# Kernel optimization log

Hardware: AMD Instinct MI355X
Metric: run time of the kernel (lower is better)

## Reference

```python
import jax, jax.numpy as jnp
import numpy as np

DIM = 384
NUM_HEADS = 12
WS = 8            # window_size
SS = 4            # shift_size
HEAD_DIM = DIM // NUM_HEADS
SCALE = HEAD_DIM ** -0.5
N = WS * WS       # tokens per window
EPS = 1e-5
MLP_HIDDEN = 4 * DIM

# relative position index (static, matches torch buffer construction)
_coords = np.stack(np.meshgrid(np.arange(WS), np.arange(WS), indexing='ij')).reshape(2, -1)
_rel = (_coords[:, :, None] - _coords[:, None, :]).transpose(1, 2, 0)  # [N,N,2]
_rel[..., 0] += WS - 1
_rel[..., 1] += WS - 1
_rel[..., 0] *= 2 * WS - 1
RPI = jnp.asarray(_rel.sum(-1))  # [N,N] int


def layer_norm(x, g, b):
    m = x.mean(-1, keepdims=True)
    v = ((x - m) ** 2).mean(-1, keepdims=True)
    return (x - m) / jnp.sqrt(v + EPS) * g + b


def window_partition(x):
    B, Hh, Ww, C = x.shape
    x = x.reshape(B, Hh // WS, WS, Ww // WS, WS, C).transpose(0, 1, 3, 2, 4, 5)
    return x.reshape(-1, WS, WS, C)


def window_reverse(w, Hh, Ww):
    B = w.shape[0] // ((Hh // WS) * (Ww // WS))
    x = w.reshape(B, Hh // WS, Ww // WS, WS, WS, -1).transpose(0, 1, 3, 2, 4, 5)
    return x.reshape(B, Hh, Ww, -1)


def attention_mask(Hp, Wp):
    # region id along each axis: 0 = [0, Hp-WS), 1 = [Hp-WS, Hp-SS), 2 = [Hp-SS, Hp)
    h_id = np.zeros(Hp, np.int32); h_id[Hp - WS:Hp - SS] = 1; h_id[Hp - SS:] = 2
    w_id = np.zeros(Wp, np.int32); w_id[Wp - WS:Wp - SS] = 1; w_id[Wp - SS:] = 2
    cnt = h_id[:, None] * 3 + w_id[None, :]                      # [Hp, Wp]
    img = jnp.asarray(cnt, jnp.float32).reshape(1, Hp, Wp, 1)
    mw = window_partition(img).reshape(-1, N)                    # [nW, N]
    am = mw[:, None, :] - mw[:, :, None]                         # [nW, N, N]
    return jnp.where(am != 0, jnp.float32(-100.0), jnp.float32(0.0))


def setup_inputs() -> dict:
    key = jax.random.key(0)
    ks = jax.random.split(key, 8)
    B, H, W = 32, 64, 64
    std = 0.02
    return {
        'x': jax.random.normal(ks[0], (B, H * W, DIM), jnp.float32),
        'qkv_w': jax.random.normal(ks[1], (DIM, 3 * DIM), jnp.float32) * std,
        'qkv_b': jnp.zeros((3 * DIM,), jnp.float32),
        'proj_w': jax.random.normal(ks[2], (DIM, DIM), jnp.float32) * std,
        'proj_b': jnp.zeros((DIM,), jnp.float32),
        'rpb_table': jax.random.normal(ks[3], ((2 * WS - 1) * (2 * WS - 1), NUM_HEADS), jnp.float32) * std,
        'n1_g': jnp.ones((DIM,), jnp.float32), 'n1_b': jnp.zeros((DIM,), jnp.float32),
        'n2_g': jnp.ones((DIM,), jnp.float32), 'n2_b': jnp.zeros((DIM,), jnp.float32),
        'fc1_w': jax.random.normal(ks[4], (DIM, MLP_HIDDEN), jnp.float32) * std,
        'fc1_b': jnp.zeros((MLP_HIDDEN,), jnp.float32),
        'fc2_w': jax.random.normal(ks[5], (MLP_HIDDEN, DIM), jnp.float32) * std,
        'fc2_b': jnp.zeros((DIM,), jnp.float32),
        'H': 64, 'W': 64,
    }


def reference(x, qkv_w, qkv_b, proj_w, proj_b, rpb_table, n1_g, n1_b, n2_g, n2_b,
              fc1_w, fc1_b, fc2_w, fc2_b, H, W):
    B, L, C = x.shape
    shortcut = x
    h = layer_norm(x, n1_g, n1_b).reshape(B, H, W, C)
    pad_r = (WS - W % WS) % WS
    pad_b = (WS - H % WS) % WS
    if pad_r or pad_b:
        h = jnp.pad(h, ((0, 0), (0, pad_b), (0, pad_r), (0, 0)))
    Hp, Wp = H + pad_b, W + pad_r
    shifted = jnp.roll(h, shift=(-SS, -SS), axis=(1, 2))
    xw = window_partition(shifted).reshape(-1, N, C)             # [B_, N, C]
    B_ = xw.shape[0]

    qkv = (xw @ qkv_w + qkv_b).reshape(B_, N, 3, NUM_HEADS, HEAD_DIM)
    q = qkv[:, :, 0].transpose(0, 2, 1, 3) * SCALE               # [B_, h, N, d]
    k = qkv[:, :, 1].transpose(0, 2, 1, 3)
    v = qkv[:, :, 2].transpose(0, 2, 1, 3)

    attn = jnp.einsum('bhnd,bhmd->bhnm', q, k)                   # [B_, h, N, N]
    bias = rpb_table[RPI].transpose(2, 0, 1)                     # [h, N, N]
    attn = attn + bias[None]

    mask = attention_mask(Hp, Wp)                                # [nW, N, N]
    nW = mask.shape[0]
    attn = attn.reshape(B_ // nW, nW, NUM_HEADS, N, N) + mask[None, :, None]
    attn = jax.nn.softmax(attn.reshape(B_, NUM_HEADS, N, N), axis=-1)

    out = jnp.einsum('bhnm,bhmd->bhnd', attn, v)
    out = out.transpose(0, 2, 1, 3).reshape(B_, N, C)
    out = out @ proj_w + proj_b

    out = window_reverse(out.reshape(-1, WS, WS, C), Hp, Wp)
    out = jnp.roll(out, shift=(SS, SS), axis=(1, 2))
    out = out[:, :H, :W, :].reshape(B, H * W, C)

    x = shortcut + out
    h2 = layer_norm(x, n2_g, n2_b)
    mlp = jax.nn.gelu(h2 @ fc1_w + fc1_b, approximate=False) @ fc2_w + fc2_b
    return x + mlp
```

## Files before the change

kernel.cpp:

```cpp
#include <hip/hip_runtime.h>
#include <math.h>


#define ROWS_TOTAL 131072
#define NWIN_TOTAL 2048

typedef __attribute__((ext_vector_type(8))) __bf16 bf16x8;
typedef __attribute__((ext_vector_type(4))) float f32x4;
typedef __attribute__((ext_vector_type(8))) unsigned short ushort8;

__device__ __forceinline__ unsigned short f2bf(float f) {
  unsigned u = __builtin_bit_cast(unsigned, f);
  u = (u + 0x7fffu + ((u >> 16) & 1u)) >> 16;
  return (unsigned short)u;
}
__device__ __forceinline__ float bf2f(unsigned short u) {
  return __builtin_bit_cast(float, (unsigned)u << 16);
}

__device__ __forceinline__ void gload16(const void* g, void* l) {
  __builtin_amdgcn_global_load_lds(
      (const __attribute__((address_space(1))) unsigned int*)g,
      (__attribute__((address_space(3))) unsigned int*)l, 16, 0, 0);
}

__device__ __forceinline__ int gather_row(int win, int t) {
  int b = win >> 6, wi = (win >> 3) & 7, wj = win & 7;
  int gi = (wi * 8 + (t >> 3) + 4) & 63;
  int gj = (wj * 8 + (t & 7) + 4) & 63;
  return (b << 12) + (gi << 6) + gj;
}

__device__ __forceinline__ float gelu_f(float v) {
  float x = v * 0.70710678118654752f;
  float ax = fabsf(x);
  float t = 1.f / (1.f + 0.3275911f * ax);
  float poly =
      t * (0.254829592f +
           t * (-0.284496736f +
                t * (1.421413741f + t * (-1.453152027f + t * 1.061405429f))));
  float er = 1.f - poly * __expf(-x * x);
  er = copysignf(er, x);
  return 0.5f * v * (1.f + er);
}

#define STG(buf_, t_)                                                   \
  {                                                                     \
    size_t ko = (size_t)(t_) * 64;                                      \
    gload16(aS0 + ko, (char*)As + (buf_) * 8192 + tid * 16);            \
    gload16(aS1 + ko, (char*)As + (buf_) * 8192 + 4096 + tid * 16);     \
    gload16(bS0 + ko, (char*)Bs + (buf_) * 6144 + tid * 16);            \
    if (tid < 128)                                                      \
      gload16(bS1 + ko, (char*)Bs + (buf_) * 6144 + 4096 + tid * 16);   \
  }

#define GEMM_DECLS()                                                    \
  f32x4 acc[4][3];                                                      \
  _Pragma("unroll") for (int i_ = 0; i_ < 4; ++i_)                      \
  _Pragma("unroll") for (int j_ = 0; j_ < 3; ++j_)                      \
      acc[i_][j_] = (f32x4)(0.f);                                       \
  int aO[4], bO[3];                                                     \
  _Pragma("unroll") for (int mi_ = 0; mi_ < 4; ++mi_) {                 \
    int row_ = wr * 64 + mi_ * 16 + lr;                                 \
    aO[mi_] = row_ * 32 + (((hi + (row_ >> 1)) & 3) << 3);              \
  }                                                                     \
  _Pragma("unroll") for (int nj_ = 0; nj_ < 3; ++nj_) {                 \
    int row_ = wc * 48 + nj_ * 16 + lr;                                 \
    bO[nj_] = row_ * 32 + (((hi + (row_ >> 1)) & 3) << 3);              \
  }

#define GEMM_CORE(NT_)                                                  \
  {                                                                     \
    int cur = 0;                                                        \
    STG(0, 0);                                                          \
    __syncthreads();                                                    \
    for (int t = 0; t < (NT_); ++t) {                                   \
      if (t + 1 < (NT_)) STG(cur ^ 1, t + 1);                           \
      const ushort* AsC = &As[cur][0];                                  \
      const ushort* BsC = &Bs[cur][0];                                  \
      bf16x8 bv[3];                                                     \
      _Pragma("unroll") for (int nj = 0; nj < 3; ++nj)                  \
          bv[nj] = *(const bf16x8*)(BsC + bO[nj]);                      \
      _Pragma("unroll") for (int mi = 0; mi < 4; ++mi) {                \
        bf16x8 av = *(const bf16x8*)(AsC + aO[mi]);                     \
        _Pragma("unroll") for (int nj = 0; nj < 3; ++nj)                \
          acc[mi][nj] = __builtin_amdgcn_mfma_f32_16x16x32_bf16(        \
              av, bv[nj], acc[mi][nj], 0, 0, 0);                        \
      }                                                                 \
      __syncthreads();                                                  \
      cur ^= 1;                                                         \
    }                                                                   \
  }

#define GRID_SWZ(NP_)                                                   \
  int p, bm;                                                            \
  {                                                                     \
    int lin = blockIdx.y * (NP_) + blockIdx.x;                          \
    if ((gridDim.y & 7) == 0) {                                         \
      int xcd = lin & 7, q = lin >> 3;                                  \
      p = q % (NP_); bm = (q / (NP_)) * 8 + xcd;                        \
    } else { p = blockIdx.x; bm = blockIdx.y; }                         \
  }

#define SRC_SWZ(t_) (((((t_) & 3) - (((t_) >> 3) & 3)) & 3) << 4)

__global__ __launch_bounds__(256) void wprep_k(
    const float* __restrict__ qkvw, const float* __restrict__ projw,
    const float* __restrict__ fc1w, const float* __restrict__ fc2w,
    ushort* __restrict__ wq, ushort* __restrict__ wp,
    ushort* __restrict__ w1, ushort* __restrict__ w2) {
  int gid = blockIdx.x * 256 + threadIdx.x;
  const int S1 = 1152 * 384;
  const int S2 = S1 + 384 * 384;
  const int S3 = S2 + 1536 * 384;
  const int S4 = S3 + 384 * 1536;
  if (gid < S1) {
    int n = gid / 384, k = gid - n * 384;
    wq[gid] = f2bf(qkvw[(size_t)k * 1152 + n]);
  } else if (gid < S2) {
    int i = gid - S1, n = i / 384, k = i - n * 384;
    wp[i] = f2bf(projw[(size_t)k * 384 + n]);
  } else if (gid < S3) {
    int i = gid - S2, n = i / 384, k = i - n * 384;
    w1[i] = f2bf(fc1w[(size_t)k * 1536 + n]);
  } else if (gid < S4) {
    int i = gid - S3, n = i / 1536, k = i - n * 1536;
    w2[i] = f2bf(fc2w[(size_t)k * 384 + n]);
  }
}

__global__ __launch_bounds__(256) void ln_fused_k(
    const float* __restrict__ x, const float* __restrict__ g,
    const float* __restrict__ b, ushort* __restrict__ o) {
  int wid = threadIdx.x >> 6, lane = threadIdx.x & 63;
  int row = (blockIdx.x << 2) + wid;
  const float* p = x + (size_t)row * 384;
  float2 v[3];
  float s = 0.f, ss = 0.f;
#pragma unroll
  for (int c = 0; c < 3; ++c) {
    v[c] = *(const float2*)(p + lane * 2 + c * 128);
    s += v[c].x + v[c].y;
    ss += v[c].x * v[c].x + v[c].y * v[c].y;
  }
#pragma unroll
  for (int off = 1; off < 64; off <<= 1) {
    s += __shfl_xor(s, off);
    ss += __shfl_xor(ss, off);
  }
  float m = s * (1.f / 384.f);
  float r = rsqrtf(ss * (1.f / 384.f) - m * m + 1e-5f);
  ushort* op = o + (size_t)row * 384;
#pragma unroll
  for (int c = 0; c < 3; ++c) {
    float2 gg = *(const float2*)(g + lane * 2 + c * 128);
    float2 bb = *(const float2*)(b + lane * 2 + c * 128);
    union { ushort u[2]; unsigned w; } pk;
    pk.u[0] = f2bf((v[c].x - m) * r * gg.x + bb.x);
    pk.u[1] = f2bf((v[c].y - m) * r * gg.y + bb.y);
    *(unsigned*)(op + lane * 2 + c * 128) = pk.w;
  }
}

__global__ __launch_bounds__(256) void qkv_mfma_k(
    const ushort* __restrict__ xln, const ushort* __restrict__ wq,
    const float* __restrict__ qkvb, ushort* __restrict__ qd,
    ushort* __restrict__ kd, ushort* __restrict__ vd, int wc0) {
  __shared__ __align__(16) ushort As[2][4096];
  __shared__ __align__(16) ushort Bs[2][3072];
  const int tid = threadIdx.x;
  const int lane = tid & 63;
  const int w = tid >> 6;
  const int wr = w >> 1, wc = w & 1;
  const int lr = lane & 15, hi = lane >> 4;
  GRID_SWZ(12);
  const int n0 = p * 96;
  int r0 = tid >> 2, r1 = (256 + tid) >> 2;
  const char* aS0 = (const char*)xln +
                    (size_t)gather_row(wc0 + bm * 2 + (r0 >> 6), r0 & 63) * 768 +
                    SRC_SWZ(tid);
  const char* aS1 = (const char*)xln +
                    (size_t)gather_row(wc0 + bm * 2 + (r1 >> 6), r1 & 63) * 768 +
                    SRC_SWZ(tid);
  const char* bS0 = (const char*)wq + (size_t)(n0 + (tid >> 2)) * 768 +
                    SRC_SWZ(tid);
  const char* bS1 = (const char*)wq + (size_t)(n0 + 64 + (tid >> 2)) * 768 +
                    SRC_SWZ(tid);
  GEMM_DECLS();
  GEMM_CORE(12);
  const float scale = 0.17677669529663687f;
#pragma unroll
  for (int mi = 0; mi < 4; ++mi) {
#pragma unroll
    for (int r = 0; r < 4; ++r) {
      int rr = wr * 64 + mi * 16 + (hi << 2) + r;
      int w_rel = bm * 2 + (rr >> 6), t = rr & 63;
#pragma unroll
      for (int nj = 0; nj < 3; ++nj) {
        int nc = n0 + wc * 48 + nj * 16 + lr;
        float v = acc[mi][nj][r] + qkvb[nc];
        int qi = nc / 384, rem = nc - qi * 384;
        int hh = rem >> 5, d = rem & 31;
        ushort* base = (qi == 0) ? qd : (qi == 1 ? kd : vd);
        if (qi == 0) v *= scale;
        base[(((size_t)w_rel * 12 + hh) << 11) + (t << 5) + d] = f2bf(v);
      }
    }
  }
}

__global__ __launch_bounds__(128) void attn_k(
    const ushort* __restrict__ q, const ushort* __restrict__ k,
    const ushort* __restrict__ v, const float* __restrict__ rpb,
    ushort* __restrict__ ao, int wc0) {
  __shared__ __align__(16) float kbuf[2][64][32];
  __shared__ __align__(16) float vbuf[2][64][32];
  __shared__ float bias[2][232];
  __shared__ int region[64];
  const int tid = threadIdx.x;
  const int wid = tid >> 6, lane = tid & 63;
  const int w = blockIdx.x, win = wc0 + w;
  const int head = blockIdx.y * 2 + wid;
  if (tid < 64) {
    int wi = (win >> 3) & 7, wj = win & 7;
    int pi = wi * 8 + (tid >> 3), pj = wj * 8 + (tid & 7);
    int ri = pi < 56 ? 0 : (pi < 60 ? 1 : 2);
    int rj = pj < 56 ? 0 : (pj < 60 ? 1 : 2);
    region[tid] = ri * 3 + rj;
  }
  const size_t hb = ((size_t)w * 12 + head) * 2048;
  const ushort* kp = k + hb;
  const ushort* vp = v + hb;
#pragma unroll
  for (int s = 0; s < 4; ++s) {
    int f = s * 64 + lane;
    int r = f >> 2, c = (f & 3) * 8;
    ushort8 ku = *(const ushort8*)(kp + r * 32 + c);
    ushort8 vu = *(const ushort8*)(vp + r * 32 + c);
#pragma unroll
    for (int j = 0; j < 8; ++j) {
      kbuf[wid][r][c + j] = bf2f(ku[j]);
      vbuf[wid][r][c + j] = bf2f(vu[j]);
    }
  }
  for (int s = lane; s < 225; s += 64) bias[wid][s] = rpb[s * 12 + head];
  __syncthreads();
  const int i = lane;
  float qr[32];
  const ushort* qp = q + hb + (i << 5);
#pragma unroll
  for (int c = 0; c < 4; ++c) {
    ushort8 qu = *(const ushort8*)(qp + c * 8);
#pragma unroll
    for (int j = 0; j < 8; ++j) qr[c * 8 + j] = bf2f(qu[j]);
  }
  const int yi = i >> 3, xi = i & 7, regi = region[i];
  float sc[64];
  float mx = -3.0e38f;
#pragma unroll
  for (int j = 0; j < 64; ++j) {
    float a = 0.f;
#pragma unroll
    for (int c = 0; c < 32; c += 4) {
      float4 kv = *(float4*)&kbuf[wid][j][c];
      a = fmaf(qr[c], kv.x, a);
      a = fmaf(qr[c + 1], kv.y, a);
      a = fmaf(qr[c + 2], kv.z, a);
      a = fmaf(qr[c + 3], kv.w, a);
    }
    int dy = yi - (j >> 3) + 7, dx = xi - (j & 7) + 7;
    a += bias[wid][dy * 15 + dx];
    if (region[j] != regi) a -= 100.f;
    sc[j] = a;
    mx = fmaxf(mx, a);
  }
  float sum = 0.f;
#pragma unroll
  for (int j = 0; j < 64; ++j) {
    float e = __expf(sc[j] - mx);
    sc[j] = e;
    sum += e;
  }
  const float inv = 1.f / sum;
  float o[32];
#pragma unroll
  for (int c = 0; c < 32; ++c) o[c] = 0.f;
#pragma unroll
  for (int j = 0; j < 64; ++j) {
    float p = sc[j];
#pragma unroll
    for (int c = 0; c < 32; c += 4) {
      float4 vv = *(float4*)&vbuf[wid][j][c];
      o[c] = fmaf(p, vv.x, o[c]);
      o[c + 1] = fmaf(p, vv.y, o[c + 1]);
      o[c + 2] = fmaf(p, vv.z, o[c + 2]);
      o[c + 3] = fmaf(p, vv.w, o[c + 3]);
    }
  }
  ushort* op = ao + ((size_t)(w * 64 + i)) * 384 + (head << 5);
#pragma unroll
  for (int c = 0; c < 32; c += 8) {
    ushort8 pk;
#pragma unroll
    for (int j2 = 0; j2 < 8; ++j2) pk[j2] = f2bf(o[c + j2] * inv);
    *(ushort8*)(op + c) = pk;
  }
}

__global__ __launch_bounds__(256) void proj_mfma_k(
    const ushort* __restrict__ ao, const ushort* __restrict__ wp,
    const float* __restrict__ pb, const float* __restrict__ x,
    float* __restrict__ x2, int wc0) {
  __shared__ __align__(16) ushort As[2][4096];
  __shared__ __align__(16) ushort Bs[2][3072];
  const int tid = threadIdx.x;
  const int lane = tid & 63;
  const int w = tid >> 6;
  const int wr = w >> 1, wc = w & 1;
  const int lr = lane & 15, hi = lane >> 4;
  GRID_SWZ(4);
  const int n0 = p * 96;
  const char* aS0 = (const char*)ao +
                    (size_t)(bm * 128 + (tid >> 2)) * 768 + SRC_SWZ(tid);
  const char* aS1 = (const char*)ao +
                    (size_t)(bm * 128 + 64 + (tid >> 2)) * 768 + SRC_SWZ(tid);
  const char* bS0 = (const char*)wp + (size_t)(n0 + (tid >> 2)) * 768 +
                    SRC_SWZ(tid);
  const char* bS1 = (const char*)wp + (size_t)(n0 + 64 + (tid >> 2)) * 768 +
                    SRC_SWZ(tid);
  GEMM_DECLS();
  GEMM_CORE(12);
#pragma unroll
  for (int mi = 0; mi < 4; ++mi) {
#pragma unroll
    for (int r = 0; r < 4; ++r) {
      int rr = wr * 64 + mi * 16 + (hi << 2) + r;
      int gl = bm * 128 + rr;
      int gr = gather_row(wc0 + (gl >> 6), gl & 63);
#pragma unroll
      for (int nj = 0; nj < 3; ++nj) {
        int nc = n0 + wc * 48 + nj * 16 + lr;
        size_t idx = (size_t)gr * 384 + nc;
        x2[idx] = acc[mi][nj][r] + pb[nc] + x[idx];
      }
    }
  }
}

__global__ __launch_bounds__(256) void fc1_mfma_k(
    const ushort* __restrict__ x2ln, const ushort* __restrict__ w1,
    const float* __restrict__ fb, ushort* __restrict__ hm, int row0) {
  __shared__ __align__(16) ushort As[2][4096];
  __shared__ __align__(16) ushort Bs[2][3072];
  const int tid = threadIdx.x;
  const int lane = tid & 63;
  const int w = tid >> 6;
  const int wr = w >> 1, wc = w & 1;
  const int lr = lane & 15, hi = lane >> 4;
  GRID_SWZ(16);
  const int n0 = p * 96;
  const char* aS0 = (const char*)x2ln +
                    (size_t)(row0 + bm * 128 + (tid >> 2)) * 768 +
                    SRC_SWZ(tid);
  const char* aS1 = (const char*)x2ln +
                    (size_t)(row0 + bm * 128 + 64 + (tid >> 2)) * 768 +
                    SRC_SWZ(tid);
  const char* bS0 = (const char*)w1 + (size_t)(n0 + (tid >> 2)) * 768 +
                    SRC_SWZ(tid);
  const char* bS1 = (const char*)w1 + (size_t)(n0 + 64 + (tid >> 2)) * 768 +
                    SRC_SWZ(tid);
  GEMM_DECLS();
  GEMM_CORE(12);
#pragma unroll
  for (int mi = 0; mi < 4; ++mi) {
#pragma unroll
    for (int r = 0; r < 4; ++r) {
      int rr = wr * 64 + mi * 16 + (hi << 2) + r;
      size_t lrow = (size_t)(bm * 128 + rr);
#pragma unroll
      for (int nj = 0; nj < 3; ++nj) {
        int nc = n0 + wc * 48 + nj * 16 + lr;
        float v = gelu_f(acc[mi][nj][r] + fb[nc]);
        hm[lrow * 1536 + nc] = f2bf(v);
      }
    }
  }
}

__global__ __launch_bounds__(256) void fc2_mfma_k(
    const ushort* __restrict__ hm, const ushort* __restrict__ w2,
    const float* __restrict__ fb, float* __restrict__ out, int row0) {
  __shared__ __align__(16) ushort As[2][4096];
  __shared__ __align__(16) ushort Bs[2][3072];
  const int tid = threadIdx.x;
  const int lane = tid & 63;
  const int w = tid >> 6;
  const int wr = w >> 1, wc = w & 1;
  const int lr = lane & 15, hi = lane >> 4;
  GRID_SWZ(4);
  const int n0 = p * 96;
  const char* aS0 = (const char*)hm +
                    (size_t)(bm * 128 + (tid >> 2)) * 3072 + SRC_SWZ(tid);
  const char* aS1 = (const char*)hm +
                    (size_t)(bm * 128 + 64 + (tid >> 2)) * 3072 +
                    SRC_SWZ(tid);
  const char* bS0 = (const char*)w2 + (size_t)(n0 + (tid >> 2)) * 3072 +
                    SRC_SWZ(tid);
  const char* bS1 = (const char*)w2 + (size_t)(n0 + 64 + (tid >> 2)) * 3072 +
                    SRC_SWZ(tid);
  GEMM_DECLS();
  GEMM_CORE(48);
#pragma unroll
  for (int mi = 0; mi < 4; ++mi) {
#pragma unroll
    for (int r = 0; r < 4; ++r) {
      int rr = wr * 64 + mi * 16 + (hi << 2) + r;
      size_t grow = (size_t)(row0 + bm * 128 + rr);
#pragma unroll
      for (int nj = 0; nj < 3; ++nj) {
        int nc = n0 + wc * 48 + nj * 16 + lr;
        size_t idx = grow * 384 + nc;
        out[idx] = out[idx] + acc[mi][nj][r] + fb[nc];
      }
    }
  }
}

extern "C" void kernel_launch(void* const* d_in, const int* in_sizes, int n_in,
                              void* d_out, int out_size, void* d_ws, size_t ws_size,
                              hipStream_t stream) {
  const float* x = (const float*)d_in[0];
  const float* qkv_w = (const float*)d_in[1];
  const float* qkv_b = (const float*)d_in[2];
  const float* proj_w = (const float*)d_in[3];
  const float* proj_b = (const float*)d_in[4];
  const float* rpb = (const float*)d_in[5];
  const float* n1g = (const float*)d_in[6];
  const float* n1b = (const float*)d_in[7];
  const float* n2g = (const float*)d_in[8];
  const float* n2b = (const float*)d_in[9];
  const float* fc1w = (const float*)d_in[10];
  const float* fc1b = (const float*)d_in[11];
  const float* fc2w = (const float*)d_in[12];
  const float* fc2b = (const float*)d_in[13];
  float* out = (float*)d_out;
  char* ws = (char*)d_ws;

  ushort* wq = (ushort*)ws;
  ushort* wp = wq + 442368;
  ushort* w1 = wp + 147456;
  ushort* w2 = w1 + 589824;
  ushort* xln = (ushort*)(ws + 3538944);
  char* scratch = ws + 3538944 + 100663296;
  size_t base = 3538944 + 100663296;
  size_t ssz = (ws_size > base) ? ws_size - base : 0;

  wprep_k<<<6912, 256, 0, stream>>>(qkv_w, proj_w, fc1w, fc2w, wq, wp, w1, w2);
  ln_fused_k<<<ROWS_TOTAL / 4, 256, 0, stream>>>(x, n1g, n1b, xln);

  const size_t perwin = 196608;
  int nwc = (int)(ssz / perwin);
  if (nwc > NWIN_TOTAL) nwc = NWIN_TOTAL;
  nwc &= ~31;
  if (nwc < 32) nwc = 32;
  ushort* qd = (ushort*)scratch;
  ushort* kd = qd + (size_t)nwc * 24576;
  ushort* vd = kd + (size_t)nwc * 24576;
  ushort* ao = vd + (size_t)nwc * 24576;
  for (int wc0 = 0; wc0 < NWIN_TOTAL; wc0 += nwc) {
    int nw = (NWIN_TOTAL - wc0 < nwc) ? (NWIN_TOTAL - wc0) : nwc;
    qkv_mfma_k<<<dim3(12, nw / 2), 256, 0, stream>>>(xln, wq, qkv_b, qd, kd,
                                                     vd, wc0);
    attn_k<<<dim3(nw, 6), 128, 0, stream>>>(qd, kd, vd, rpb, ao, wc0);
    proj_mfma_k<<<dim3(4, nw / 2), 256, 0, stream>>>(ao, wp, proj_b, x, out,
                                                     wc0);
  }

  ln_fused_k<<<ROWS_TOTAL / 4, 256, 0, stream>>>(out, n2g, n2b, xln);
  const size_t pergrp = 393216;
  int ngc = (int)(ssz / pergrp);
  if (ngc > 1024) ngc = 1024;
  ngc &= ~7;
  if (ngc < 8) ngc = 8;
  ushort* hm = (ushort*)scratch;
  for (int g0 = 0; g0 < 1024; g0 += ngc) {
    int ng = (1024 - g0 < ngc) ? (1024 - g0) : ngc;
    fc1_mfma_k<<<dim3(16, ng), 256, 0, stream>>>(xln, w1, fc1b, hm, g0 * 128);
    fc2_mfma_k<<<dim3(4, ng), 256, 0, stream>>>(hm, w2, fc2b, out, g0 * 128);
  }
}
```

Measured before the change: 1.552 ms.

## Switch GEMMs to 32x32x16 MFMA with 128x192 block tiles

All four GEMM kernels (qkv, proj, fc1, fc2) move from 16x16x32 MFMA to 32x32x16 MFMA with 16-float accumulators. The block N tile doubles from 96 to 192 columns, so B staging in LDS grows and the grid's N dimension is halved. The goal is higher arithmetic intensity per LDS read and fewer A-tile reloads across N blocks. In exchange there is more LDS per block and more accumulator registers, which may lower occupancy, and the epilogues now use a different output row mapping.

```diff
diff --git a/kernel.cpp b/kernel.cpp
--- a/kernel.cpp
+++ b/kernel.cpp
@@ -6,7 +6,7 @@
 #define NWIN_TOTAL 2048
 
 typedef __attribute__((ext_vector_type(8))) __bf16 bf16x8;
-typedef __attribute__((ext_vector_type(4))) float f32x4;
+typedef __attribute__((ext_vector_type(16))) float f32x16;
 typedef __attribute__((ext_vector_type(8))) unsigned short ushort8;
 
 __device__ __forceinline__ unsigned short f2bf(float f) {
@@ -44,29 +44,37 @@
   return 0.5f * v * (1.f + er);
 }
 
+#define SRC_SWZ(t_) (((((t_) & 3) - (((t_) >> 3) & 3)) & 3) << 4)
+
 #define STG(buf_, t_)                                                   \
   {                                                                     \
     size_t ko = (size_t)(t_) * 64;                                      \
     gload16(aS0 + ko, (char*)As + (buf_) * 8192 + tid * 16);            \
     gload16(aS1 + ko, (char*)As + (buf_) * 8192 + 4096 + tid * 16);     \
-    gload16(bS0 + ko, (char*)Bs + (buf_) * 6144 + tid * 16);            \
-    if (tid < 128)                                                      \
-      gload16(bS1 + ko, (char*)Bs + (buf_) * 6144 + 4096 + tid * 16);   \
+    gload16(bS0 + ko, (char*)Bs + (buf_) * 12288 + tid * 16);           \
+    gload16(bS1 + ko, (char*)Bs + (buf_) * 12288 + 4096 + tid * 16);    \
+    gload16(bS2 + ko, (char*)Bs + (buf_) * 12288 + 8192 + tid * 16);    \
   }
 
 #define GEMM_DECLS()                                                    \
-  f32x4 acc[4][3];                                                      \
-  _Pragma("unroll") for (int i_ = 0; i_ < 4; ++i_)                      \
+  f32x16 acc[2][3];                                                     \
+  _Pragma("unroll") for (int i_ = 0; i_ < 2; ++i_)                      \
   _Pragma("unroll") for (int j_ = 0; j_ < 3; ++j_)                      \
-      acc[i_][j_] = (f32x4)(0.f);                                       \
-  int aO[4], bO[3];                                                     \
-  _Pragma("unroll") for (int mi_ = 0; mi_ < 4; ++mi_) {                 \
-    int row_ = wr * 64 + mi_ * 16 + lr;                                 \
-    aO[mi_] = row_ * 32 + (((hi + (row_ >> 1)) & 3) << 3);              \
+      acc[i_][j_] = (f32x16)(0.f);                                      \
+  int aO[2][2], bO[3][2];                                               \
+  _Pragma("unroll") for (int mi_ = 0; mi_ < 2; ++mi_) {                 \
+    int row_ = wr * 64 + mi_ * 32 + (lane & 31);                        \
+    _Pragma("unroll") for (int sl_ = 0; sl_ < 2; ++sl_) {               \
+      int g_ = sl_ * 2 + (lane >> 5);                                   \
+      aO[mi_][sl_] = row_ * 32 + (((g_ + (row_ >> 1)) & 3) << 3);       \
+    }                                                                   \
   }                                                                     \
   _Pragma("unroll") for (int nj_ = 0; nj_ < 3; ++nj_) {                 \
-    int row_ = wc * 48 + nj_ * 16 + lr;                                 \
-    bO[nj_] = row_ * 32 + (((hi + (row_ >> 1)) & 3) << 3);              \
+    int row_ = wc * 96 + nj_ * 32 + (lane & 31);                        \
+    _Pragma("unroll") for (int sl_ = 0; sl_ < 2; ++sl_) {               \
+      int g_ = sl_ * 2 + (lane >> 5);                                   \
+      bO[nj_][sl_] = row_ * 32 + (((g_ + (row_ >> 1)) & 3) << 3);       \
+    }                                                                   \
   }
 
 #define GEMM_CORE(NT_)                                                  \
@@ -78,15 +86,18 @@
       if (t + 1 < (NT_)) STG(cur ^ 1, t + 1);                           \
       const ushort* AsC = &As[cur][0];                                  \
       const ushort* BsC = &Bs[cur][0];                                  \
-      bf16x8 bv[3];                                                     \
+      bf16x8 av[2][2], bv[3][2];                                        \
+      _Pragma("unroll") for (int mi = 0; mi < 2; ++mi)                  \
+      _Pragma("unroll") for (int sl = 0; sl < 2; ++sl)                  \
+          av[mi][sl] = *(const bf16x8*)(AsC + aO[mi][sl]);              \
       _Pragma("unroll") for (int nj = 0; nj < 3; ++nj)                  \
-          bv[nj] = *(const bf16x8*)(BsC + bO[nj]);                      \
-      _Pragma("unroll") for (int mi = 0; mi < 4; ++mi) {                \
-        bf16x8 av = *(const bf16x8*)(AsC + aO[mi]);                     \
-        _Pragma("unroll") for (int nj = 0; nj < 3; ++nj)                \
-          acc[mi][nj] = __builtin_amdgcn_mfma_f32_16x16x32_bf16(        \
-              av, bv[nj], acc[mi][nj], 0, 0, 0);                        \
-      }                                                                 \
+      _Pragma("unroll") for (int sl = 0; sl < 2; ++sl)                  \
+          bv[nj][sl] = *(const bf16x8*)(BsC + bO[nj][sl]);              \
+      _Pragma("unroll") for (int sl = 0; sl < 2; ++sl)                  \
+      _Pragma("unroll") for (int mi = 0; mi < 2; ++mi)                  \
+      _Pragma("unroll") for (int nj = 0; nj < 3; ++nj)                  \
+          acc[mi][nj] = __builtin_amdgcn_mfma_f32_32x32x16_bf16(        \
+              av[mi][sl], bv[nj][sl], acc[mi][nj], 0, 0, 0);            \
       __syncthreads();                                                  \
       cur ^= 1;                                                         \
     }                                                                   \
@@ -102,7 +113,7 @@
     } else { p = blockIdx.x; bm = blockIdx.y; }                         \
   }
 
-#define SRC_SWZ(t_) (((((t_) & 3) - (((t_) >> 3) & 3)) & 3) << 4)
+#define CD_ROW(r_, lane_) (((r_) & 3) + 8 * ((r_) >> 2) + 4 * ((lane_) >> 5))
 
 __global__ __launch_bounds__(256) void wprep_k(
     const float* __restrict__ qkvw, const float* __restrict__ projw,
@@ -167,15 +178,14 @@
     const float* __restrict__ qkvb, ushort* __restrict__ qd,
     ushort* __restrict__ kd, ushort* __restrict__ vd, int wc0) {
   __shared__ __align__(16) ushort As[2][4096];
-  __shared__ __align__(16) ushort Bs[2][3072];
+  __shared__ __align__(16) ushort Bs[2][6144];
   const int tid = threadIdx.x;
   const int lane = tid & 63;
   const int w = tid >> 6;
   const int wr = w >> 1, wc = w & 1;
-  const int lr = lane & 15, hi = lane >> 4;
-  GRID_SWZ(12);
-  const int n0 = p * 96;
-  int r0 = tid >> 2, r1 = (256 + tid) >> 2;
+  GRID_SWZ(6);
+  const int n0 = p * 192;
+  int r0 = tid >> 2, r1 = 64 + (tid >> 2);
   const char* aS0 = (const char*)xln +
                     (size_t)gather_row(wc0 + bm * 2 + (r0 >> 6), r0 & 63) * 768 +
                     SRC_SWZ(tid);
@@ -185,19 +195,21 @@
   const char* bS0 = (const char*)wq + (size_t)(n0 + (tid >> 2)) * 768 +
                     SRC_SWZ(tid);
   const char* bS1 = (const char*)wq + (size_t)(n0 + 64 + (tid >> 2)) * 768 +
+                    SRC_SWZ(tid);
+  const char* bS2 = (const char*)wq + (size_t)(n0 + 128 + (tid >> 2)) * 768 +
                     SRC_SWZ(tid);
   GEMM_DECLS();
   GEMM_CORE(12);
   const float scale = 0.17677669529663687f;
 #pragma unroll
-  for (int mi = 0; mi < 4; ++mi) {
-#pragma unroll
-    for (int r = 0; r < 4; ++r) {
-      int rr = wr * 64 + mi * 16 + (hi << 2) + r;
+  for (int mi = 0; mi < 2; ++mi) {
+#pragma unroll
+    for (int r = 0; r < 16; ++r) {
+      int rr = wr * 64 + mi * 32 + CD_ROW(r, lane);
       int w_rel = bm * 2 + (rr >> 6), t = rr & 63;
 #pragma unroll
       for (int nj = 0; nj < 3; ++nj) {
-        int nc = n0 + wc * 48 + nj * 16 + lr;
+        int nc = n0 + wc * 96 + nj * 32 + (lane & 31);
         float v = acc[mi][nj][r] + qkvb[nc];
         int qi = nc / 384, rem = nc - qi * 384;
         int hh = rem >> 5, d = rem & 31;
@@ -312,14 +324,13 @@
     const float* __restrict__ pb, const float* __restrict__ x,
     float* __restrict__ x2, int wc0) {
   __shared__ __align__(16) ushort As[2][4096];
-  __shared__ __align__(16) ushort Bs[2][3072];
+  __shared__ __align__(16) ushort Bs[2][6144];
   const int tid = threadIdx.x;
   const int lane = tid & 63;
   const int w = tid >> 6;
   const int wr = w >> 1, wc = w & 1;
-  const int lr = lane & 15, hi = lane >> 4;
-  GRID_SWZ(4);
-  const int n0 = p * 96;
+  GRID_SWZ(2);
+  const int n0 = p * 192;
   const char* aS0 = (const char*)ao +
                     (size_t)(bm * 128 + (tid >> 2)) * 768 + SRC_SWZ(tid);
   const char* aS1 = (const char*)ao +
@@ -328,18 +339,20 @@
                     SRC_SWZ(tid);
   const char* bS1 = (const char*)wp + (size_t)(n0 + 64 + (tid >> 2)) * 768 +
                     SRC_SWZ(tid);
+  const char* bS2 = (const char*)wp + (size_t)(n0 + 128 + (tid >> 2)) * 768 +
+                    SRC_SWZ(tid);
   GEMM_DECLS();
   GEMM_CORE(12);
 #pragma unroll
-  for (int mi = 0; mi < 4; ++mi) {
-#pragma unroll
-    for (int r = 0; r < 4; ++r) {
-      int rr = wr * 64 + mi * 16 + (hi << 2) + r;
+  for (int mi = 0; mi < 2; ++mi) {
+#pragma unroll
+    for (int r = 0; r < 16; ++r) {
+      int rr = wr * 64 + mi * 32 + CD_ROW(r, lane);
       int gl = bm * 128 + rr;
       int gr = gather_row(wc0 + (gl >> 6), gl & 63);
 #pragma unroll
       for (int nj = 0; nj < 3; ++nj) {
-        int nc = n0 + wc * 48 + nj * 16 + lr;
+        int nc = n0 + wc * 96 + nj * 32 + (lane & 31);
         size_t idx = (size_t)gr * 384 + nc;
         x2[idx] = acc[mi][nj][r] + pb[nc] + x[idx];
       }
@@ -351,14 +364,13 @@
     const ushort* __restrict__ x2ln, const ushort* __restrict__ w1,
     const float* __restrict__ fb, ushort* __restrict__ hm, int row0) {
   __shared__ __align__(16) ushort As[2][4096];
-  __shared__ __align__(16) ushort Bs[2][3072];
+  __shared__ __align__(16) ushort Bs[2][6144];
   const int tid = threadIdx.x;
   const int lane = tid & 63;
   const int w = tid >> 6;
   const int wr = w >> 1, wc = w & 1;
-  const int lr = lane & 15, hi = lane >> 4;
-  GRID_SWZ(16);
-  const int n0 = p * 96;
+  GRID_SWZ(8);
+  const int n0 = p * 192;
   const char* aS0 = (const char*)x2ln +
                     (size_t)(row0 + bm * 128 + (tid >> 2)) * 768 +
                     SRC_SWZ(tid);
@@ -369,17 +381,18 @@
                     SRC_SWZ(tid);
   const char* bS1 = (const char*)w1 + (size_t)(n0 + 64 + (tid >> 2)) * 768 +
                     SRC_SWZ(tid);
+  const char* bS2 = (const char*)w1 + (size_t)(n0 + 128 + (tid >> 2)) * 768 +
+                    SRC_SWZ(tid);
   GEMM_DECLS();
   GEMM_CORE(12);
 #pragma unroll
-  for (int mi = 0; mi < 4; ++mi) {
-#pragma unroll
-    for (int r = 0; r < 4; ++r) {
-      int rr = wr * 64 + mi * 16 + (hi << 2) + r;
-      size_t lrow = (size_t)(bm * 128 + rr);
+  for (int mi = 0; mi < 2; ++mi) {
+#pragma unroll
+    for (int r = 0; r < 16; ++r) {
+      size_t lrow = (size_t)(bm * 128 + wr * 64 + mi * 32 + CD_ROW(r, lane));
 #pragma unroll
       for (int nj = 0; nj < 3; ++nj) {
-        int nc = n0 + wc * 48 + nj * 16 + lr;
+        int nc = n0 + wc * 96 + nj * 32 + (lane & 31);
         float v = gelu_f(acc[mi][nj][r] + fb[nc]);
         hm[lrow * 1536 + nc] = f2bf(v);
       }
@@ -391,14 +404,13 @@
     const ushort* __restrict__ hm, const ushort* __restrict__ w2,
     const float* __restrict__ fb, float* __restrict__ out, int row0) {
   __shared__ __align__(16) ushort As[2][4096];
-  __shared__ __align__(16) ushort Bs[2][3072];
+  __shared__ __align__(16) ushort Bs[2][6144];
   const int tid = threadIdx.x;
   const int lane = tid & 63;
   const int w = tid >> 6;
   const int wr = w >> 1, wc = w & 1;
-  const int lr = lane & 15, hi = lane >> 4;
-  GRID_SWZ(4);
-  const int n0 = p * 96;
+  GRID_SWZ(2);
+  const int n0 = p * 192;
   const char* aS0 = (const char*)hm +
                     (size_t)(bm * 128 + (tid >> 2)) * 3072 + SRC_SWZ(tid);
   const char* aS1 = (const char*)hm +
@@ -408,17 +420,19 @@
                     SRC_SWZ(tid);
   const char* bS1 = (const char*)w2 + (size_t)(n0 + 64 + (tid >> 2)) * 3072 +
                     SRC_SWZ(tid);
+  const char* bS2 = (const char*)w2 + (size_t)(n0 + 128 + (tid >> 2)) * 3072 +
+                    SRC_SWZ(tid);
   GEMM_DECLS();
   GEMM_CORE(48);
 #pragma unroll
-  for (int mi = 0; mi < 4; ++mi) {
-#pragma unroll
-    for (int r = 0; r < 4; ++r) {
-      int rr = wr * 64 + mi * 16 + (hi << 2) + r;
-      size_t grow = (size_t)(row0 + bm * 128 + rr);
+  for (int mi = 0; mi < 2; ++mi) {
+#pragma unroll
+    for (int r = 0; r < 16; ++r) {
+      size_t grow =
+          (size_t)(row0 + bm * 128 + wr * 64 + mi * 32 + CD_ROW(r, lane));
 #pragma unroll
       for (int nj = 0; nj < 3; ++nj) {
-        int nc = n0 + wc * 48 + nj * 16 + lr;
+        int nc = n0 + wc * 96 + nj * 32 + (lane & 31);
         size_t idx = grow * 384 + nc;
         out[idx] = out[idx] + acc[mi][nj][r] + fb[nc];
       }
@@ -469,10 +483,10 @@
   ushort* ao = vd + (size_t)nwc * 24576;
   for (int wc0 = 0; wc0 < NWIN_TOTAL; wc0 += nwc) {
     int nw = (NWIN_TOTAL - wc0 < nwc) ? (NWIN_TOTAL - wc0) : nwc;
-    qkv_mfma_k<<<dim3(12, nw / 2), 256, 0, stream>>>(xln, wq, qkv_b, qd, kd,
-                                                     vd, wc0);
+    qkv_mfma_k<<<dim3(6, nw / 2), 256, 0, stream>>>(xln, wq, qkv_b, qd, kd,
+                                                    vd, wc0);
     attn_k<<<dim3(nw, 6), 128, 0, stream>>>(qd, kd, vd, rpb, ao, wc0);
-    proj_mfma_k<<<dim3(4, nw / 2), 256, 0, stream>>>(ao, wp, proj_b, x, out,
+    proj_mfma_k<<<dim3(2, nw / 2), 256, 0, stream>>>(ao, wp, proj_b, x, out,
                                                      wc0);
   }
 
@@ -485,7 +499,7 @@
   ushort* hm = (ushort*)scratch;
   for (int g0 = 0; g0 < 1024; g0 += ngc) {
     int ng = (1024 - g0 < ngc) ? (1024 - g0) : ngc;
-    fc1_mfma_k<<<dim3(16, ng), 256, 0, stream>>>(xln, w1, fc1b, hm, g0 * 128);
-    fc2_mfma_k<<<dim3(4, ng), 256, 0, stream>>>(hm, w2, fc2b, out, g0 * 128);
-  }
-}
+    fc1_mfma_k<<<dim3(8, ng), 256, 0, stream>>>(xln, w1, fc1b, hm, g0 * 128);
+    fc2_mfma_k<<<dim3(2, ng), 256, 0, stream>>>(hm, w2, fc2b, out, g0 * 128);
+  }
+}
```

Result: slower. 1.609 ms (+3.7%).
